# Optimization experiments

Hardware: AMD Instinct MI355X
Metric: run time of the kernel (lower is better)

Reference implementation:

```python
import jax, jax.numpy as jnp
import numpy as np

N_NODES = 50000
N_EDGES = 800000
IN_NODE = 64
IN_EDGE = 64
HIDDEN = 128
OUT_NODE = 64


def _linear_params(key, fan_in, fan_out):
    k1, k2 = jax.random.split(key)
    bound = 1.0 / np.sqrt(fan_in)
    W = jax.random.uniform(k1, (fan_out, fan_in), jnp.float32, -bound, bound)
    b = jax.random.uniform(k2, (fan_out,), jnp.float32, -bound, bound)
    return W, b


def setup_inputs() -> dict:
    key = jax.random.key(0)
    ks = jax.random.split(key, 10)
    src_node_features = jax.random.normal(ks[0], (N_NODES, IN_NODE), jnp.float32)
    edge_index = jax.random.randint(ks[1], (2, N_EDGES), 0, N_NODES, dtype=jnp.int32).astype(jnp.int64)
    edge_attr = jax.random.normal(ks[2], (N_EDGES, IN_EDGE), jnp.float32)
    u = jax.random.normal(ks[3], (1, 16), jnp.float32)
    batch = jnp.zeros((N_NODES,), jnp.int64)
    # node_mlp_1: Linear(in_node+in_edge, hidden) -> ReLU -> Linear(hidden, out)
    W1a, b1a = _linear_params(ks[4], IN_NODE + IN_EDGE, HIDDEN)
    W1b, b1b = _linear_params(ks[5], HIDDEN, OUT_NODE)
    # node_mlp_2: Linear(in_node+out, hidden) -> ReLU -> Linear(hidden, out)
    W2a, b2a = _linear_params(ks[6], IN_NODE + OUT_NODE, HIDDEN)
    W2b, b2b = _linear_params(ks[7], HIDDEN, OUT_NODE)
    # residual_combine: Linear(out+in_node, out)
    Wr, br = _linear_params(ks[8], OUT_NODE + IN_NODE, OUT_NODE)
    return {
        "src_node_features": src_node_features,
        "edge_index": edge_index,
        "edge_attr": edge_attr,
        "u": u,
        "batch": batch,
        "W1a": W1a, "b1a": b1a, "W1b": W1b, "b1b": b1b,
        "W2a": W2a, "b2a": b2a, "W2b": W2b, "b2b": b2b,
        "Wr": Wr, "br": br,
    }


def reference(src_node_features, edge_index, edge_attr, u, batch,
              W1a, b1a, W1b, b1b, W2a, b2a, W2b, b2b, Wr, br):
    n_nodes = src_node_features.shape[0]
    row, col = edge_index[0], edge_index[1]
    # gather source-node features per edge and concat with edge features: [E, in_node+in_edge]
    msg = jnp.concatenate([src_node_features[col], edge_attr], axis=1)
    # node_mlp_1
    h = jax.nn.relu(msg @ W1a.T + b1a)
    h = h @ W1b.T + b1b  # [E, out]
    # scatter_mean over destination nodes (row)
    sums = jax.ops.segment_sum(h, row, num_segments=n_nodes)
    counts = jax.ops.segment_sum(jnp.ones((h.shape[0],), h.dtype), row, num_segments=n_nodes)
    agg = sums / jnp.maximum(counts, 1.0)[:, None]  # [N, out]
    # node_mlp_2
    z = jnp.concatenate([src_node_features, agg], axis=1)
    z = jax.nn.relu(z @ W2a.T + b2a)
    z = z @ W2b.T + b2b  # [N, out]
    # residual combine
    out = jnp.concatenate([z, src_node_features], axis=1) @ Wr.T + br
    return out
```

## Files before the change

kernel.cpp:

```cpp
#include <hip/hip_runtime.h>

#define N_NODES 50000
#define N_EDGES 800000
#define HPAD 136
#define ZPAD 72
#define MAXDEG 64
#define ETILE 32

typedef __attribute__((ext_vector_type(8))) short short8;
typedef __attribute__((ext_vector_type(4))) float float4v;

__device__ __forceinline__ unsigned short f2bf(float x) {
    unsigned int u = __float_as_uint(x);
    u += 0x7fff + ((u >> 16) & 1);
    return (unsigned short)(u >> 16);
}
__device__ __forceinline__ float bf2f(unsigned short b) {
    return __uint_as_float(((unsigned int)b) << 16);
}
__device__ __forceinline__ int clampN(int v) {
    v = v < 0 ? 0 : v;
    return v >= N_NODES ? N_NODES - 1 : v;
}
__device__ __forceinline__ short8 cvt8(const float* __restrict__ p) {
    float4v f0 = *reinterpret_cast<const float4v*>(p);
    float4v f1 = *reinterpret_cast<const float4v*>(p + 4);
    short8 v;
    #pragma unroll
    for (int j = 0; j < 4; ++j) {
        v[j]     = (short)f2bf(f0[j]);
        v[j + 4] = (short)f2bf(f1[j]);
    }
    return v;
}
__device__ __forceinline__ int loadIdx(const int* __restrict__ p, long i, bool w64) {
    return w64 ? p[2 * i] : p[i];
}
__device__ __forceinline__ bool idxIs64(const int* __restrict__ p) {
    return (p[1] | p[3] | p[5] | p[7]) == 0;
}

#define OFF_W1A 0
#define OFF_W1B 16384
#define OFF_W2A 24576
#define OFF_W2B 40960
#define OFF_WR  49152
#define WBF_TOT 57344

__global__ void wcvt_kernel(const float* __restrict__ W1a, const float* __restrict__ W1b,
                            const float* __restrict__ W2a, const float* __restrict__ W2b,
                            const float* __restrict__ Wr, unsigned short* __restrict__ wbf)
{
    int i = blockIdx.x * 256 + threadIdx.x;
    if (i >= WBF_TOT) return;
    float v;
    if      (i < OFF_W1B) v = W1a[i - OFF_W1A];
    else if (i < OFF_W2A) v = W1b[i - OFF_W1B];
    else if (i < OFF_W2B) v = W2a[i - OFF_W2A];
    else if (i < OFF_WR)  v = W2b[i - OFF_W2B];
    else                  v = Wr[i - OFF_WR];
    wbf[i] = f2bf(v);
}

__global__ void scvt_kernel(const float* __restrict__ src, unsigned short* __restrict__ sbf)
{
    int i = blockIdx.x * 256 + threadIdx.x;
    sbf[i] = f2bf(src[i]);
}

__global__ __launch_bounds__(256, 2)
void edge_kernel5(const float* __restrict__ src,
                  const int* __restrict__ eidx,
                  const float* __restrict__ eattr,
                  const unsigned short* __restrict__ wbf,
                  const unsigned short* __restrict__ srcbf,
                  const float* __restrict__ b1a,
                  const float* __restrict__ b1b,
                  unsigned short* __restrict__ h,
                  int* __restrict__ cnt,
                  int* __restrict__ adj)
{
    __shared__ __align__(16) unsigned short h_lds[4][ETILE][HPAD];

    const int tid  = threadIdx.x;
    const int wave = tid >> 6;
    const int lane = tid & 63;
    const int quad = lane >> 4;
    const int lm   = lane & 15;
    const int ebase = blockIdx.x * (ETILE * 4) + wave * ETILE;

    const bool w64 = idxIs64(eidx);

    if (lane < ETILE) {
        const int e = ebase + lane;
        const int r = clampN(loadIdx(eidx, e, w64));
        const int pos = atomicAdd(&cnt[r], 1);
        if (pos < MAXDEG) adj[r * MAXDEG + pos] = e;
    }

    int col[2];
    #pragma unroll
    for (int t = 0; t < 2; ++t)
        col[t] = clampN(loadIdx(eidx, (long)N_EDGES + ebase + t * 16 + lm, w64));

    short8 a1[2][4];
    if (srcbf) {
        #pragma unroll
        for (int t = 0; t < 2; ++t) {
            #pragma unroll
            for (int s = 0; s < 2; ++s)
                a1[t][s] = *reinterpret_cast<const short8*>(
                    srcbf + (long)col[t] * 64 + s * 32 + quad * 8);
            #pragma unroll
            for (int s = 2; s < 4; ++s)
                a1[t][s] = cvt8(eattr + (long)(ebase + t * 16 + lm) * 64 + (s - 2) * 32 + quad * 8);
        }
    } else {
        #pragma unroll
        for (int t = 0; t < 2; ++t) {
            #pragma unroll
            for (int s = 0; s < 4; ++s) {
                const int kb = s * 32 + quad * 8;
                const float* p = (s < 2) ? (src + (long)col[t] * 64 + kb)
                                         : (eattr + (long)(ebase + t * 16 + lm) * 64 + (kb - 64));
                a1[t][s] = cvt8(p);
            }
        }
    }

    const unsigned short* W1a = wbf + OFF_W1A;
    const unsigned short* W1b = wbf + OFF_W1B;

    #pragma unroll
    for (int nt = 0; nt < 8; ++nt) {
        short8 bfr[4];
        #pragma unroll
        for (int s = 0; s < 4; ++s)
            bfr[s] = *reinterpret_cast<const short8*>(W1a + (nt * 16 + lm) * 128 + s * 32 + quad * 8);
        float4v acc0 = {0.f, 0.f, 0.f, 0.f};
        float4v acc1 = {0.f, 0.f, 0.f, 0.f};
        #pragma unroll
        for (int s = 0; s < 4; ++s) {
            acc0 = __builtin_amdgcn_mfma_f32_16x16x32_bf16(a1[0][s], bfr[s], acc0, 0, 0, 0);
            acc1 = __builtin_amdgcn_mfma_f32_16x16x32_bf16(a1[1][s], bfr[s], acc1, 0, 0, 0);
        }
        const float bias = b1a[nt * 16 + lm];
        #pragma unroll
        for (int r = 0; r < 4; ++r) {
            float v0 = acc0[r] + bias; v0 = v0 > 0.f ? v0 : 0.f;
            float v1 = acc1[r] + bias; v1 = v1 > 0.f ? v1 : 0.f;
            h_lds[wave][quad * 4 + r][nt * 16 + lm]      = f2bf(v0);
            h_lds[wave][16 + quad * 4 + r][nt * 16 + lm] = f2bf(v1);
        }
    }

    short8 a2[2][4];
    #pragma unroll
    for (int t = 0; t < 2; ++t)
        #pragma unroll
        for (int s = 0; s < 4; ++s)
            a2[t][s] = *reinterpret_cast<const short8*>(&h_lds[wave][t * 16 + lm][s * 32 + quad * 8]);

    #pragma unroll
    for (int nt = 0; nt < 4; ++nt) {
        short8 bfr[4];
        #pragma unroll
        for (int s = 0; s < 4; ++s)
            bfr[s] = *reinterpret_cast<const short8*>(W1b + (nt * 16 + lm) * 128 + s * 32 + quad * 8);
        float4v acc0 = {0.f, 0.f, 0.f, 0.f};
        float4v acc1 = {0.f, 0.f, 0.f, 0.f};
        #pragma unroll
        for (int s = 0; s < 4; ++s) {
            acc0 = __builtin_amdgcn_mfma_f32_16x16x32_bf16(a2[0][s], bfr[s], acc0, 0, 0, 0);
            acc1 = __builtin_amdgcn_mfma_f32_16x16x32_bf16(a2[1][s], bfr[s], acc1, 0, 0, 0);
        }
        const float bias = b1b[nt * 16 + lm];
        #pragma unroll
        for (int r = 0; r < 4; ++r) {
            h_lds[wave][quad * 4 + r][nt * 16 + lm]      = f2bf(acc0[r] + bias);
            h_lds[wave][16 + quad * 4 + r][nt * 16 + lm] = f2bf(acc1[r] + bias);
        }
    }

    const int m    = lane >> 1;
    const int half = lane & 1;
    #pragma unroll
    for (int i = 0; i < 2; ++i) {
        short8 v = *reinterpret_cast<const short8*>(&h_lds[wave][m][half * 32 + i * 16 + 0]);
        short8 w = *reinterpret_cast<const short8*>(&h_lds[wave][m][half * 32 + i * 16 + 8]);
        unsigned short* g = h + (long)(ebase + m) * 64 + half * 32 + i * 16;
        *reinterpret_cast<short8*>(g)     = v;
        *reinterpret_cast<short8*>(g + 8) = w;
    }
}

__global__ __launch_bounds__(256, 8)
void agg_kernel(const unsigned short* __restrict__ h,
                const int* __restrict__ cnt,
                const int* __restrict__ adj,
                unsigned short* __restrict__ aggbf)
{
    const int tid  = threadIdx.x;
    const int wave = tid >> 6;
    const int lane = tid & 63;
    const int g = lane >> 3;
    const int s = lane & 7;
    const int n = blockIdx.x * 4 + wave;

    const int deg  = cnt[n];
    const int degc = deg > MAXDEG ? MAXDEG : deg;
    const int* arow = adj + n * MAXDEG;

    float acc[8];
    #pragma unroll
    for (int c = 0; c < 8; ++c) acc[c] = 0.f;

    for (int j = g; j < degc; j += 8) {
        const int e = arow[j];
        short8 v = *reinterpret_cast<const short8*>(h + (long)e * 64 + s * 8);
        #pragma unroll
        for (int c = 0; c < 8; ++c) acc[c] += bf2f((unsigned short)v[c]);
    }

    #pragma unroll
    for (int m = 8; m < 64; m <<= 1) {
        #pragma unroll
        for (int c = 0; c < 8; ++c)
            acc[c] += __shfl_xor(acc[c], m, 64);
    }

    if (g == 0) {
        const float inv = 1.f / (deg > 1 ? (float)deg : 1.f);
        short8 o;
        #pragma unroll
        for (int c = 0; c < 8; ++c) o[c] = (short)f2bf(acc[c] * inv);
        *reinterpret_cast<short8*>(aggbf + (long)n * 64 + s * 8) = o;
    }
}

__global__ __launch_bounds__(256, 2)
void node_mlp_kernel(const unsigned short* __restrict__ srcbf,
                     const unsigned short* __restrict__ aggbf,
                     const unsigned short* __restrict__ wbf,
                     const float* __restrict__ b2a,
                     const float* __restrict__ b2b,
                     const float* __restrict__ br,
                     float* __restrict__ out)
{
    __shared__ __align__(16) unsigned short h_lds[4][16][HPAD];
    __shared__ __align__(16) unsigned short z_lds[4][16][ZPAD];

    const int tid  = threadIdx.x;
    const int wave = tid >> 6;
    const int lane = tid & 63;
    const int quad = lane >> 4;
    const int lm   = lane & 15;
    const int nbase = blockIdx.x * 64 + wave * 16;
    const int node_g = clampN(nbase + lm);

    short8 a1f[4];
    #pragma unroll
    for (int s = 0; s < 2; ++s)
        a1f[s] = *reinterpret_cast<const short8*>(srcbf + (long)node_g * 64 + s * 32 + quad * 8);
    #pragma unroll
    for (int s = 2; s < 4; ++s)
        a1f[s] = *reinterpret_cast<const short8*>(aggbf + (long)node_g * 64 + (s - 2) * 32 + quad * 8);

    const unsigned short* W2a = wbf + OFF_W2A;
    const unsigned short* W2b = wbf + OFF_W2B;
    const unsigned short* Wr  = wbf + OFF_WR;

    #pragma unroll
    for (int nt = 0; nt < 8; ++nt) {
        float4v acc = {0.f, 0.f, 0.f, 0.f};
        #pragma unroll
        for (int s = 0; s < 4; ++s) {
            short8 b = *reinterpret_cast<const short8*>(W2a + (nt * 16 + lm) * 128 + s * 32 + quad * 8);
            acc = __builtin_amdgcn_mfma_f32_16x16x32_bf16(a1f[s], b, acc, 0, 0, 0);
        }
        const float bias = b2a[nt * 16 + lm];
        #pragma unroll
        for (int r = 0; r < 4; ++r) {
            float v = acc[r] + bias;
            v = v > 0.f ? v : 0.f;
            h_lds[wave][quad * 4 + r][nt * 16 + lm] = f2bf(v);
        }
    }

    short8 a2f[4];
    #pragma unroll
    for (int s = 0; s < 4; ++s)
        a2f[s] = *reinterpret_cast<const short8*>(&h_lds[wave][lm][s * 32 + quad * 8]);

    #pragma unroll
    for (int nt = 0; nt < 4; ++nt) {
        float4v acc = {0.f, 0.f, 0.f, 0.f};
        #pragma unroll
        for (int s = 0; s < 4; ++s) {
            short8 b = *reinterpret_cast<const short8*>(W2b + (nt * 16 + lm) * 128 + s * 32 + quad * 8);
            acc = __builtin_amdgcn_mfma_f32_16x16x32_bf16(a2f[s], b, acc, 0, 0, 0);
        }
        const float bias = b2b[nt * 16 + lm];
        #pragma unroll
        for (int r = 0; r < 4; ++r)
            z_lds[wave][quad * 4 + r][nt * 16 + lm] = f2bf(acc[r] + bias);
    }

    short8 a3f[4];
    #pragma unroll
    for (int s = 0; s < 2; ++s)
        a3f[s] = *reinterpret_cast<const short8*>(&z_lds[wave][lm][s * 32 + quad * 8]);
    a3f[2] = a1f[0];
    a3f[3] = a1f[1];

    #pragma unroll
    for (int nt = 0; nt < 4; ++nt) {
        float4v acc = {0.f, 0.f, 0.f, 0.f};
        #pragma unroll
        for (int s = 0; s < 4; ++s) {
            short8 b = *reinterpret_cast<const short8*>(Wr + (nt * 16 + lm) * 128 + s * 32 + quad * 8);
            acc = __builtin_amdgcn_mfma_f32_16x16x32_bf16(a3f[s], b, acc, 0, 0, 0);
        }
        const float bias = br[nt * 16 + lm];
        #pragma unroll
        for (int r = 0; r < 4; ++r) {
            const int node = nbase + quad * 4 + r;
            if (node < N_NODES)
                out[(long)node * 64 + nt * 16 + lm] = acc[r] + bias;
        }
    }
}

__global__ __launch_bounds__(256, 2)
void node_kernel3(const float* __restrict__ src,
                  const unsigned short* __restrict__ srcbf,
                  const unsigned short* __restrict__ h,
                  const int* __restrict__ cnt,
                  const int* __restrict__ adj,
                  const unsigned short* __restrict__ wbf,
                  const float* __restrict__ b2a,
                  const float* __restrict__ b2b,
                  const float* __restrict__ br,
                  float* __restrict__ out)
{
    __shared__ __align__(16) unsigned short agg_lds[4][16][ZPAD];
    __shared__ __align__(16) unsigned short h_lds[4][16][HPAD];
    __shared__ __align__(16) unsigned short z_lds[4][16][ZPAD];

    const int tid  = threadIdx.x;
    const int wave = tid >> 6;
    const int lane = tid & 63;
    const int quad = lane >> 4;
    const int lm   = lane & 15;
    const int nbase = blockIdx.x * 64 + wave * 16;

    const int node_g = clampN(nbase + lm);

    const int deg  = cnt[node_g];
    const int degc = deg > MAXDEG ? MAXDEG : deg;
    const int ch0  = quad * 16;
    const int* arow = adj + node_g * MAXDEG;

    float s0[16];
    #pragma unroll
    for (int c = 0; c < 16; ++c) s0[c] = 0.f;

    int j = 0;
    for (; j + 4 <= degc; j += 4) {
        const int4 e4 = *reinterpret_cast<const int4*>(arow + j);
        const unsigned short* p0 = h + (long)e4.x * 64 + ch0;
        const unsigned short* p1 = h + (long)e4.y * 64 + ch0;
        const unsigned short* p2 = h + (long)e4.z * 64 + ch0;
        const unsigned short* p3 = h + (long)e4.w * 64 + ch0;
        short8 a0 = *reinterpret_cast<const short8*>(p0);
        short8 b0 = *reinterpret_cast<const short8*>(p0 + 8);
        short8 a1 = *reinterpret_cast<const short8*>(p1);
        short8 b1 = *reinterpret_cast<const short8*>(p1 + 8);
        short8 a2 = *reinterpret_cast<const short8*>(p2);
        short8 b2 = *reinterpret_cast<const short8*>(p2 + 8);
        short8 a3 = *reinterpret_cast<const short8*>(p3);
        short8 b3 = *reinterpret_cast<const short8*>(p3 + 8);
        #pragma unroll
        for (int c = 0; c < 8; ++c) {
            s0[c]     += bf2f((unsigned short)a0[c]) + bf2f((unsigned short)a1[c])
                       + bf2f((unsigned short)a2[c]) + bf2f((unsigned short)a3[c]);
            s0[c + 8] += bf2f((unsigned short)b0[c]) + bf2f((unsigned short)b1[c])
                       + bf2f((unsigned short)b2[c]) + bf2f((unsigned short)b3[c]);
        }
    }
    for (; j < degc; ++j) {
        const unsigned short* p = h + (long)arow[j] * 64 + ch0;
        short8 a = *reinterpret_cast<const short8*>(p);
        short8 b = *reinterpret_cast<const short8*>(p + 8);
        #pragma unroll
        for (int c = 0; c < 8; ++c) {
            s0[c]     += bf2f((unsigned short)a[c]);
            s0[c + 8] += bf2f((unsigned short)b[c]);
        }
    }
    const float inv = 1.f / (deg > 1 ? (float)deg : 1.f);

    #pragma unroll
    for (int k = 0; k < 8; ++k) {
        unsigned int pk = ((unsigned int)f2bf(s0[2 * k + 1] * inv) << 16)
                        | f2bf(s0[2 * k] * inv);
        *reinterpret_cast<unsigned int*>(&agg_lds[wave][lm][ch0 + 2 * k]) = pk;
    }

    short8 a1f[4];
    if (srcbf) {
        #pragma unroll
        for (int s = 0; s < 2; ++s)
            a1f[s] = *reinterpret_cast<const short8*>(srcbf + (long)node_g * 64 + s * 32 + quad * 8);
    } else {
        #pragma unroll
        for (int s = 0; s < 2; ++s)
            a1f[s] = cvt8(src + (long)node_g * 64 + s * 32 + quad * 8);
    }
    #pragma unroll
    for (int s = 2; s < 4; ++s)
        a1f[s] = *reinterpret_cast<const short8*>(&agg_lds[wave][lm][(s - 2) * 32 + quad * 8]);

    const unsigned short* W2a = wbf + OFF_W2A;
    const unsigned short* W2b = wbf + OFF_W2B;
    const unsigned short* Wr  = wbf + OFF_WR;

    #pragma unroll
    for (int nt = 0; nt < 8; ++nt) {
        float4v acc = {0.f, 0.f, 0.f, 0.f};
        #pragma unroll
        for (int s = 0; s < 4; ++s) {
            short8 b = *reinterpret_cast<const short8*>(W2a + (nt * 16 + lm) * 128 + s * 32 + quad * 8);
            acc = __builtin_amdgcn_mfma_f32_16x16x32_bf16(a1f[s], b, acc, 0, 0, 0);
        }
        const float bias = b2a[nt * 16 + lm];
        #pragma unroll
        for (int r = 0; r < 4; ++r) {
            float v = acc[r] + bias;
            v = v > 0.f ? v : 0.f;
            h_lds[wave][quad * 4 + r][nt * 16 + lm] = f2bf(v);
        }
    }

    short8 a2f[4];
    #pragma unroll
    for (int s = 0; s < 4; ++s)
        a2f[s] = *reinterpret_cast<const short8*>(&h_lds[wave][lm][s * 32 + quad * 8]);

    #pragma unroll
    for (int nt = 0; nt < 4; ++nt) {
        float4v acc = {0.f, 0.f, 0.f, 0.f};
        #pragma unroll
        for (int s = 0; s < 4; ++s) {
            short8 b = *reinterpret_cast<const short8*>(W2b + (nt * 16 + lm) * 128 + s * 32 + quad * 8);
            acc = __builtin_amdgcn_mfma_f32_16x16x32_bf16(a2f[s], b, acc, 0, 0, 0);
        }
        const float bias = b2b[nt * 16 + lm];
        #pragma unroll
        for (int r = 0; r < 4; ++r)
            z_lds[wave][quad * 4 + r][nt * 16 + lm] = f2bf(acc[r] + bias);
    }

    short8 a3f[4];
    #pragma unroll
    for (int s = 0; s < 2; ++s)
        a3f[s] = *reinterpret_cast<const short8*>(&z_lds[wave][lm][s * 32 + quad * 8]);
    a3f[2] = a1f[0];
    a3f[3] = a1f[1];

    #pragma unroll
    for (int nt = 0; nt < 4; ++nt) {
        float4v acc = {0.f, 0.f, 0.f, 0.f};
        #pragma unroll
        for (int s = 0; s < 4; ++s) {
            short8 b = *reinterpret_cast<const short8*>(Wr + (nt * 16 + lm) * 128 + s * 32 + quad * 8);
            acc = __builtin_amdgcn_mfma_f32_16x16x32_bf16(a3f[s], b, acc, 0, 0, 0);
        }
        const float bias = br[nt * 16 + lm];
        #pragma unroll
        for (int r = 0; r < 4; ++r) {
            const int node = nbase + quad * 4 + r;
            if (node < N_NODES)
                out[(long)node * 64 + nt * 16 + lm] = acc[r] + bias;
        }
    }
}

__global__ __launch_bounds__(256, 2)
void edge_kernel_fb(const float* __restrict__ src, const int* __restrict__ eidx,
                    const float* __restrict__ eattr, const float* __restrict__ W1a,
                    const float* __restrict__ b1a, const float* __restrict__ W1b,
                    const float* __restrict__ b1b, float* __restrict__ sums,
                    float* __restrict__ counts)
{
    __shared__ __align__(16) unsigned short h_lds[4][16][HPAD];
    const int tid = threadIdx.x, wave = tid >> 6, lane = tid & 63;
    const int quad = lane >> 4, lm = lane & 15;
    const int ebase = blockIdx.x * 64 + wave * 16;
    const bool w64 = idxIs64(eidx);
    const int e_a = ebase + lm;
    const int colv = clampN(loadIdx(eidx, (long)N_EDGES + e_a, w64));
    short8 a1[4];
    #pragma unroll
    for (int s = 0; s < 4; ++s) {
        const int kb = s * 32 + quad * 8;
        const float* p = (s < 2) ? (src + (long)colv * 64 + kb)
                                 : (eattr + (long)e_a * 64 + (kb - 64));
        a1[s] = cvt8(p);
    }
    #pragma unroll
    for (int nt = 0; nt < 8; ++nt) {
        float4v acc = {0.f, 0.f, 0.f, 0.f};
        #pragma unroll
        for (int s = 0; s < 4; ++s) {
            short8 b = cvt8(W1a + (nt * 16 + lm) * 128 + s * 32 + quad * 8);
            acc = __builtin_amdgcn_mfma_f32_16x16x32_bf16(a1[s], b, acc, 0, 0, 0);
        }
        const float bias = b1a[nt * 16 + lm];
        #pragma unroll
        for (int r = 0; r < 4; ++r) {
            float v = acc[r] + bias; v = v > 0.f ? v : 0.f;
            h_lds[wave][quad * 4 + r][nt * 16 + lm] = f2bf(v);
        }
    }
    __syncthreads();
    short8 a2[4];
    #pragma unroll
    for (int s = 0; s < 4; ++s)
        a2[s] = *reinterpret_cast<const short8*>(&h_lds[wave][lm][s * 32 + quad * 8]);
    int rowv[4];
    #pragma unroll
    for (int r = 0; r < 4; ++r)
        rowv[r] = clampN(loadIdx(eidx, ebase + quad * 4 + r, w64));
    #pragma unroll
    for (int nt = 0; nt < 4; ++nt) {
        float4v acc = {0.f, 0.f, 0.f, 0.f};
        #pragma unroll
        for (int s = 0; s < 4; ++s) {
            short8 b = cvt8(W1b + (nt * 16 + lm) * 128 + s * 32 + quad * 8);
            acc = __builtin_amdgcn_mfma_f32_16x16x32_bf16(a2[s], b, acc, 0, 0, 0);
        }
        const float bias = b1b[nt * 16 + lm];
        #pragma unroll
        for (int r = 0; r < 4; ++r)
            atomicAdd(&sums[(long)rowv[r] * 64 + nt * 16 + lm], acc[r] + bias);
    }
    if (lane < 16)
        atomicAdd(&counts[clampN(loadIdx(eidx, ebase + lane, w64))], 1.0f);
}

__global__ __launch_bounds__(256, 2)
void node_kernel_fb(const float* __restrict__ src, const float* __restrict__ sums,
                    const float* __restrict__ counts, const float* __restrict__ W2a,
                    const float* __restrict__ b2a, const float* __restrict__ W2b,
                    const float* __restrict__ b2b, const float* __restrict__ Wr,
                    const float* __restrict__ br, float* __restrict__ out)
{
    __shared__ __align__(16) unsigned short h_lds[4][16][HPAD];
    __shared__ __align__(16) unsigned short z_lds[4][16][ZPAD];
    const int tid = threadIdx.x, wave = tid >> 6, lane = tid & 63;
    const int quad = lane >> 4, lm = lane & 15;
    const int nbase = blockIdx.x * 64 + wave * 16;
    int node_a = nbase + lm;
    if (node_a >= N_NODES) node_a = N_NODES - 1;
    float cntv = counts[node_a];
    cntv = cntv > 1.f ? cntv : 1.f;
    const float inv = 1.f / cntv;
    short8 a1[4];
    #pragma unroll
    for (int s = 0; s < 2; ++s)
        a1[s] = cvt8(src + (long)node_a * 64 + s * 32 + quad * 8);
    #pragma unroll
    for (int s = 2; s < 4; ++s) {
        const int kb = s * 32 + quad * 8 - 64;
        const float4v* p = reinterpret_cast<const float4v*>(sums + (long)node_a * 64 + kb);
        float4v f0 = p[0], f1 = p[1];
        short8 v;
        #pragma unroll
        for (int jj = 0; jj < 4; ++jj) {
            v[jj] = (short)f2bf(f0[jj] * inv);
            v[jj + 4] = (short)f2bf(f1[jj] * inv);
        }
        a1[s] = v;
    }
    #pragma unroll
    for (int nt = 0; nt < 8; ++nt) {
        float4v acc = {0.f, 0.f, 0.f, 0.f};
        #pragma unroll
        for (int s = 0; s < 4; ++s) {
            short8 b = cvt8(W2a + (nt * 16 + lm) * 128 + s * 32 + quad * 8);
            acc = __builtin_amdgcn_mfma_f32_16x16x32_bf16(a1[s], b, acc, 0, 0, 0);
        }
        const float bias = b2a[nt * 16 + lm];
        #pragma unroll
        for (int r = 0; r < 4; ++r) {
            float v = acc[r] + bias; v = v > 0.f ? v : 0.f;
            h_lds[wave][quad * 4 + r][nt * 16 + lm] = f2bf(v);
        }
    }
    __syncthreads();
    short8 a2[4];
    #pragma unroll
    for (int s = 0; s < 4; ++s)
        a2[s] = *reinterpret_cast<const short8*>(&h_lds[wave][lm][s * 32 + quad * 8]);
    #pragma unroll
    for (int nt = 0; nt < 4; ++nt) {
        float4v acc = {0.f, 0.f, 0.f, 0.f};
        #pragma unroll
        for (int s = 0; s < 4; ++s) {
            short8 b = cvt8(W2b + (nt * 16 + lm) * 128 + s * 32 + quad * 8);
            acc = __builtin_amdgcn_mfma_f32_16x16x32_bf16(a2[s], b, acc, 0, 0, 0);
        }
        const float bias = b2b[nt * 16 + lm];
        #pragma unroll
        for (int r = 0; r < 4; ++r)
            z_lds[wave][quad * 4 + r][nt * 16 + lm] = f2bf(acc[r] + bias);
    }
    __syncthreads();
    short8 a3[4];
    #pragma unroll
    for (int s = 0; s < 2; ++s)
        a3[s] = *reinterpret_cast<const short8*>(&z_lds[wave][lm][s * 32 + quad * 8]);
    a3[2] = a1[0];
    a3[3] = a1[1];
    #pragma unroll
    for (int nt = 0; nt < 4; ++nt) {
        float4v acc = {0.f, 0.f, 0.f, 0.f};
        #pragma unroll
        for (int s = 0; s < 4; ++s) {
            short8 b = cvt8(Wr + (nt * 16 + lm) * 128 + s * 32 + quad * 8);
            acc = __builtin_amdgcn_mfma_f32_16x16x32_bf16(a3[s], b, acc, 0, 0, 0);
        }
        const float bias = br[nt * 16 + lm];
        #pragma unroll
        for (int r = 0; r < 4; ++r) {
            const int node = nbase + quad * 4 + r;
            if (node < N_NODES)
                out[(long)node * 64 + nt * 16 + lm] = acc[r] + bias;
        }
    }
}

extern "C" void kernel_launch(void* const* d_in, const int* in_sizes, int n_in,
                              void* d_out, int out_size, void* d_ws, size_t ws_size,
                              hipStream_t stream) {
    const long expect[15] = {
        3200000L, 1600000L, 51200000L, 16L, 50000L,
        16384L, 128L, 8192L, 64L,
        16384L, 128L, 8192L, 64L,
        8192L, 64L
    };
    const void* slot[15];
    for (int j = 0; j < 15; ++j) slot[j] = nullptr;
    {
        int i = 0;
        for (int j = 0; j < 15 && i < n_in; ++j)
            if ((long)in_sizes[i] == expect[j]) { slot[j] = d_in[i]; ++i; }
    }
    if (!slot[0] || !slot[1] || !slot[2] || !slot[5] || !slot[6] || !slot[7] ||
        !slot[8] || !slot[9] || !slot[10] || !slot[11] || !slot[12] ||
        !slot[13] || !slot[14]) {
        for (int j = 0; j < 15 && j < n_in; ++j) slot[j] = d_in[j];
    }

    const float* src   = (const float*)slot[0];
    const int*   eidx  = (const int*)slot[1];
    const float* eattr = (const float*)slot[2];
    const float* W1a = (const float*)slot[5];
    const float* b1a = (const float*)slot[6];
    const float* W1b = (const float*)slot[7];
    const float* b1b = (const float*)slot[8];
    const float* W2a = (const float*)slot[9];
    const float* b2a = (const float*)slot[10];
    const float* W2b = (const float*)slot[11];
    const float* b2b = (const float*)slot[12];
    const float* Wr  = (const float*)slot[13];
    const float* br  = (const float*)slot[14];
    float* out = (float*)d_out;

    const size_t hBytes   = (size_t)N_EDGES * 64 * sizeof(unsigned short);
    const size_t cntOff   = hBytes;
    const size_t cntBytes = (size_t)N_NODES * sizeof(int);
    const size_t adjOff   = cntOff + cntBytes;
    const size_t adjBytes = (size_t)N_NODES * MAXDEG * sizeof(int);
    const size_t wbfOff   = adjOff + adjBytes;
    const size_t needed2  = wbfOff + (size_t)WBF_TOT * sizeof(unsigned short);
    const size_t sbfOff   = needed2;
    const size_t sbfBytes = (size_t)N_NODES * 64 * sizeof(unsigned short);
    const size_t needed3  = sbfOff + sbfBytes;
    const size_t aggOff   = needed3;
    const size_t needed4  = aggOff + sbfBytes;

    if (ws_size >= needed2) {
        unsigned short* h = (unsigned short*)d_ws;
        int* cnt = (int*)((char*)d_ws + cntOff);
        int* adj = (int*)((char*)d_ws + adjOff);
        unsigned short* wbf = (unsigned short*)((char*)d_ws + wbfOff);
        unsigned short* sbf = nullptr;

        hipMemsetAsync(cnt, 0, cntBytes, stream);
        wcvt_kernel<<<(WBF_TOT + 255) / 256, 256, 0, stream>>>(W1a, W1b, W2a, W2b, Wr, wbf);
        if (ws_size >= needed3) {
            sbf = (unsigned short*)((char*)d_ws + sbfOff);
            scvt_kernel<<<(N_NODES * 64) / 256, 256, 0, stream>>>(src, sbf);
        }
        edge_kernel5<<<N_EDGES / (ETILE * 4), 256, 0, stream>>>(src, eidx, eattr, wbf, sbf,
                                                                b1a, b1b, h, cnt, adj);
        if (ws_size >= needed4 && sbf) {
            unsigned short* aggbf = (unsigned short*)((char*)d_ws + aggOff);
            agg_kernel<<<N_NODES / 4, 256, 0, stream>>>(h, cnt, adj, aggbf);
            node_mlp_kernel<<<(N_NODES + 63) / 64, 256, 0, stream>>>(sbf, aggbf, wbf,
                                                                     b2a, b2b, br, out);
        } else {
            node_kernel3<<<(N_NODES + 63) / 64, 256, 0, stream>>>(src, sbf, h, cnt, adj, wbf,
                                                                  b2a, b2b, br, out);
        }
        return;
    }

    const size_t needed_fb = ((size_t)N_NODES * 64 + N_NODES) * sizeof(float);
    if (ws_size < needed_fb) {
        hipMemsetAsync(d_out, 0, (size_t)out_size * sizeof(float), stream);
        return;
    }
    float* sums   = (float*)d_ws;
    float* counts = sums + (size_t)N_NODES * 64;
    hipMemsetAsync(d_ws, 0, needed_fb, stream);
    edge_kernel_fb<<<N_EDGES / 64, 256, 0, stream>>>(src, eidx, eattr,
                                                     W1a, b1a, W1b, b1b, sums, counts);
    node_kernel_fb<<<(N_NODES + 63) / 64, 256, 0, stream>>>(src, sums, counts,
                                                            W2a, b2a, W2b, b2b,
                                                            Wr, br, out);
}
```

Baseline: 558.5 us.

## Persistent software-pipelined edge kernel and unrolled batched-load aggregation

Replaces the one-tile-per-wave edge kernel with a persistent grid of 1024 blocks. Each wave strides over edge tiles and prefetches the next tile's gathered node and edge features and column indices while running the MLP on the current tile. Adjacency atomics are issued before the MLP and committed after it. The aggregation kernel now issues all eight neighbour loads up front instead of looping with dependent loads, which adds memory-level parallelism at the cost of extra registers. Launch bounds change to 4 blocks per SM and node_mlp_kernel is only moved, not changed.

Result: slower. 703.6 us (+26.0%).

```diff
diff --git a/kernel.cpp b/kernel.cpp
--- a/kernel.cpp
+++ b/kernel.cpp
@@ -6,6 +6,9 @@
 #define ZPAD 72
 #define MAXDEG 64
 #define ETILE 32
+#define TILES_TOTAL 25000
+#define EDGE_BLOCKS 1024
+#define EDGE_STRIDE (EDGE_BLOCKS * 4)
 
 typedef __attribute__((ext_vector_type(8))) short short8;
 typedef __attribute__((ext_vector_type(4))) float float4v;
@@ -68,6 +71,309 @@
     sbf[i] = f2bf(src[i]);
 }
 
+__global__ __launch_bounds__(256, 4)
+void edge_kernel6(const int* __restrict__ eidx,
+                  const float* __restrict__ eattr,
+                  const unsigned short* __restrict__ wbf,
+                  const unsigned short* __restrict__ srcbf,
+                  const float* __restrict__ b1a,
+                  const float* __restrict__ b1b,
+                  unsigned short* __restrict__ h,
+                  int* __restrict__ cnt,
+                  int* __restrict__ adj)
+{
+    __shared__ __align__(16) unsigned short h_lds[4][ETILE][HPAD];
+
+    const int tid  = threadIdx.x;
+    const int wave = tid >> 6;
+    const int lane = tid & 63;
+    const int quad = lane >> 4;
+    const int lm   = lane & 15;
+    const int wg   = blockIdx.x * 4 + wave;
+
+    const bool w64 = idxIs64(eidx);
+
+    const unsigned short* W1a = wbf + OFF_W1A;
+    const unsigned short* W1b = wbf + OFF_W1B;
+
+    auto loadcols = [&](int tile, int col[2]) {
+        #pragma unroll
+        for (int t = 0; t < 2; ++t)
+            col[t] = clampN(loadIdx(eidx, (long)N_EDGES + tile * ETILE + t * 16 + lm, w64));
+    };
+    auto gather = [&](int tile, const int col[2], short8 a[2][4]) {
+        #pragma unroll
+        for (int t = 0; t < 2; ++t) {
+            #pragma unroll
+            for (int s = 0; s < 2; ++s)
+                a[t][s] = *reinterpret_cast<const short8*>(
+                    srcbf + (long)col[t] * 64 + s * 32 + quad * 8);
+            #pragma unroll
+            for (int s = 2; s < 4; ++s)
+                a[t][s] = cvt8(eattr + (long)(tile * ETILE + t * 16 + lm) * 64
+                               + (s - 2) * 32 + quad * 8);
+        }
+    };
+    auto adj_issue = [&](int tile, int& pos, int& r) {
+        pos = MAXDEG; r = 0;
+        if (lane < ETILE) {
+            r = clampN(loadIdx(eidx, tile * ETILE + lane, w64));
+            pos = atomicAdd(&cnt[r], 1);
+        }
+    };
+    auto adj_commit = [&](int tile, int pos, int r) {
+        if (lane < ETILE && pos < MAXDEG)
+            adj[r * MAXDEG + pos] = tile * ETILE + lane;
+    };
+    auto mlp_store = [&](int tile, short8 a1[2][4]) {
+        const int ebase = tile * ETILE;
+        #pragma unroll
+        for (int nt = 0; nt < 8; ++nt) {
+            short8 bfr[4];
+            #pragma unroll
+            for (int s = 0; s < 4; ++s)
+                bfr[s] = *reinterpret_cast<const short8*>(
+                    W1a + (nt * 16 + lm) * 128 + s * 32 + quad * 8);
+            float4v acc0 = {0.f, 0.f, 0.f, 0.f};
+            float4v acc1 = {0.f, 0.f, 0.f, 0.f};
+            #pragma unroll
+            for (int s = 0; s < 4; ++s) {
+                acc0 = __builtin_amdgcn_mfma_f32_16x16x32_bf16(a1[0][s], bfr[s], acc0, 0, 0, 0);
+                acc1 = __builtin_amdgcn_mfma_f32_16x16x32_bf16(a1[1][s], bfr[s], acc1, 0, 0, 0);
+            }
+            const float bias = b1a[nt * 16 + lm];
+            #pragma unroll
+            for (int r = 0; r < 4; ++r) {
+                float v0 = acc0[r] + bias; v0 = v0 > 0.f ? v0 : 0.f;
+                float v1 = acc1[r] + bias; v1 = v1 > 0.f ? v1 : 0.f;
+                h_lds[wave][quad * 4 + r][nt * 16 + lm]      = f2bf(v0);
+                h_lds[wave][16 + quad * 4 + r][nt * 16 + lm] = f2bf(v1);
+            }
+        }
+        short8 a2[2][4];
+        #pragma unroll
+        for (int t = 0; t < 2; ++t)
+            #pragma unroll
+            for (int s = 0; s < 4; ++s)
+                a2[t][s] = *reinterpret_cast<const short8*>(
+                    &h_lds[wave][t * 16 + lm][s * 32 + quad * 8]);
+        #pragma unroll
+        for (int nt = 0; nt < 4; ++nt) {
+            short8 bfr[4];
+            #pragma unroll
+            for (int s = 0; s < 4; ++s)
+                bfr[s] = *reinterpret_cast<const short8*>(
+                    W1b + (nt * 16 + lm) * 128 + s * 32 + quad * 8);
+            float4v acc0 = {0.f, 0.f, 0.f, 0.f};
+            float4v acc1 = {0.f, 0.f, 0.f, 0.f};
+            #pragma unroll
+            for (int s = 0; s < 4; ++s) {
+                acc0 = __builtin_amdgcn_mfma_f32_16x16x32_bf16(a2[0][s], bfr[s], acc0, 0, 0, 0);
+                acc1 = __builtin_amdgcn_mfma_f32_16x16x32_bf16(a2[1][s], bfr[s], acc1, 0, 0, 0);
+            }
+            const float bias = b1b[nt * 16 + lm];
+            #pragma unroll
+            for (int r = 0; r < 4; ++r) {
+                h_lds[wave][quad * 4 + r][nt * 16 + lm]      = f2bf(acc0[r] + bias);
+                h_lds[wave][16 + quad * 4 + r][nt * 16 + lm] = f2bf(acc1[r] + bias);
+            }
+        }
+        const int m    = lane >> 1;
+        const int half = lane & 1;
+        #pragma unroll
+        for (int i = 0; i < 2; ++i) {
+            short8 v = *reinterpret_cast<const short8*>(&h_lds[wave][m][half * 32 + i * 16 + 0]);
+            short8 w = *reinterpret_cast<const short8*>(&h_lds[wave][m][half * 32 + i * 16 + 8]);
+            unsigned short* g = h + (long)(ebase + m) * 64 + half * 32 + i * 16;
+            *reinterpret_cast<short8*>(g)     = v;
+            *reinterpret_cast<short8*>(g + 8) = w;
+        }
+    };
+
+    short8 A[2][4], B[2][4];
+    int colN[2], colNN[2];
+
+    const int t0 = wg;
+    {
+        int cols0[2];
+        loadcols(t0, cols0);
+        int pos0, r0;
+        adj_issue(t0, pos0, r0);
+        gather(t0, cols0, A);
+        if (t0 + EDGE_STRIDE < TILES_TOTAL) loadcols(t0 + EDGE_STRIDE, colN);
+        adj_commit(t0, pos0, r0);
+    }
+
+    for (int t = t0; t < TILES_TOTAL; t += EDGE_STRIDE) {
+        const int tn  = t + EDGE_STRIDE;
+        const int tnn = t + 2 * EDGE_STRIDE;
+        if (tnn < TILES_TOTAL) loadcols(tnn, colNN);
+        int posB = MAXDEG, rB = 0;
+        if (tn < TILES_TOTAL) {
+            gather(tn, colN, B);
+            adj_issue(tn, posB, rB);
+        }
+        mlp_store(t, A);
+        if (tn < TILES_TOTAL) {
+            adj_commit(tn, posB, rB);
+            #pragma unroll
+            for (int x = 0; x < 2; ++x) {
+                #pragma unroll
+                for (int s = 0; s < 4; ++s) A[x][s] = B[x][s];
+                colN[x] = colNN[x];
+            }
+        }
+    }
+}
+
+__global__ __launch_bounds__(256, 4)
+void agg_kernel2(const unsigned short* __restrict__ h,
+                 const int* __restrict__ cnt,
+                 const int* __restrict__ adj,
+                 unsigned short* __restrict__ aggbf)
+{
+    const int tid  = threadIdx.x;
+    const int wave = tid >> 6;
+    const int lane = tid & 63;
+    const int g = lane >> 3;
+    const int s = lane & 7;
+    const int n = blockIdx.x * 4 + wave;
+
+    const int deg  = cnt[n];
+    const int degc = deg > MAXDEG ? MAXDEG : deg;
+    const int* arow = adj + n * MAXDEG;
+
+    int e[8];
+    #pragma unroll
+    for (int k = 0; k < 8; ++k) {
+        const int j = g + k * 8;
+        e[k] = (j < degc) ? arow[j] : -1;
+    }
+    short8 v[8];
+    #pragma unroll
+    for (int k = 0; k < 8; ++k) {
+        short8 z = {0, 0, 0, 0, 0, 0, 0, 0};
+        v[k] = z;
+        if (e[k] >= 0)
+            v[k] = *reinterpret_cast<const short8*>(h + (long)e[k] * 64 + s * 8);
+    }
+    float acc[8];
+    #pragma unroll
+    for (int c = 0; c < 8; ++c) acc[c] = 0.f;
+    #pragma unroll
+    for (int k = 0; k < 8; ++k)
+        #pragma unroll
+        for (int c = 0; c < 8; ++c) acc[c] += bf2f((unsigned short)v[k][c]);
+
+    #pragma unroll
+    for (int m = 8; m < 64; m <<= 1) {
+        #pragma unroll
+        for (int c = 0; c < 8; ++c)
+            acc[c] += __shfl_xor(acc[c], m, 64);
+    }
+
+    if (g == 0) {
+        const float inv = 1.f / (deg > 1 ? (float)deg : 1.f);
+        short8 o;
+        #pragma unroll
+        for (int c = 0; c < 8; ++c) o[c] = (short)f2bf(acc[c] * inv);
+        *reinterpret_cast<short8*>(aggbf + (long)n * 64 + s * 8) = o;
+    }
+}
+
+__global__ __launch_bounds__(256, 2)
+void node_mlp_kernel(const unsigned short* __restrict__ srcbf,
+                     const unsigned short* __restrict__ aggbf,
+                     const unsigned short* __restrict__ wbf,
+                     const float* __restrict__ b2a,
+                     const float* __restrict__ b2b,
+                     const float* __restrict__ br,
+                     float* __restrict__ out)
+{
+    __shared__ __align__(16) unsigned short h_lds[4][16][HPAD];
+    __shared__ __align__(16) unsigned short z_lds[4][16][ZPAD];
+
+    const int tid  = threadIdx.x;
+    const int wave = tid >> 6;
+    const int lane = tid & 63;
+    const int quad = lane >> 4;
+    const int lm   = lane & 15;
+    const int nbase = blockIdx.x * 64 + wave * 16;
+    const int node_g = clampN(nbase + lm);
+
+    short8 a1f[4];
+    #pragma unroll
+    for (int s = 0; s < 2; ++s)
+        a1f[s] = *reinterpret_cast<const short8*>(srcbf + (long)node_g * 64 + s * 32 + quad * 8);
+    #pragma unroll
+    for (int s = 2; s < 4; ++s)
+        a1f[s] = *reinterpret_cast<const short8*>(aggbf + (long)node_g * 64 + (s - 2) * 32 + quad * 8);
+
+    const unsigned short* W2a = wbf + OFF_W2A;
+    const unsigned short* W2b = wbf + OFF_W2B;
+    const unsigned short* Wr  = wbf + OFF_WR;
+
+    #pragma unroll
+    for (int nt = 0; nt < 8; ++nt) {
+        float4v acc = {0.f, 0.f, 0.f, 0.f};
+        #pragma unroll
+        for (int s = 0; s < 4; ++s) {
+            short8 b = *reinterpret_cast<const short8*>(W2a + (nt * 16 + lm) * 128 + s * 32 + quad * 8);
+            acc = __builtin_amdgcn_mfma_f32_16x16x32_bf16(a1f[s], b, acc, 0, 0, 0);
+        }
+        const float bias = b2a[nt * 16 + lm];
+        #pragma unroll
+        for (int r = 0; r < 4; ++r) {
+            float v = acc[r] + bias;
+            v = v > 0.f ? v : 0.f;
+            h_lds[wave][quad * 4 + r][nt * 16 + lm] = f2bf(v);
+        }
+    }
+
+    short8 a2f[4];
+    #pragma unroll
+    for (int s = 0; s < 4; ++s)
+        a2f[s] = *reinterpret_cast<const short8*>(&h_lds[wave][lm][s * 32 + quad * 8]);
+
+    #pragma unroll
+    for (int nt = 0; nt < 4; ++nt) {
+        float4v acc = {0.f, 0.f, 0.f, 0.f};
+        #pragma unroll
+        for (int s = 0; s < 4; ++s) {
+            short8 b = *reinterpret_cast<const short8*>(W2b + (nt * 16 + lm) * 128 + s * 32 + quad * 8);
+            acc = __builtin_amdgcn_mfma_f32_16x16x32_bf16(a2f[s], b, acc, 0, 0, 0);
+        }
+        const float bias = b2b[nt * 16 + lm];
+        #pragma unroll
+        for (int r = 0; r < 4; ++r)
+            z_lds[wave][quad * 4 + r][nt * 16 + lm] = f2bf(acc[r] + bias);
+    }
+
+    short8 a3f[4];
+    #pragma unroll
+    for (int s = 0; s < 2; ++s)
+        a3f[s] = *reinterpret_cast<const short8*>(&z_lds[wave][lm][s * 32 + quad * 8]);
+    a3f[2] = a1f[0];
+    a3f[3] = a1f[1];
+
+    #pragma unroll
+    for (int nt = 0; nt < 4; ++nt) {
+        float4v acc = {0.f, 0.f, 0.f, 0.f};
+        #pragma unroll
+        for (int s = 0; s < 4; ++s) {
+            short8 b = *reinterpret_cast<const short8*>(Wr + (nt * 16 + lm) * 128 + s * 32 + quad * 8);
+            acc = __builtin_amdgcn_mfma_f32_16x16x32_bf16(a3f[s], b, acc, 0, 0, 0);
+        }
+        const float bias = br[nt * 16 + lm];
+        #pragma unroll
+        for (int r = 0; r < 4; ++r) {
+            const int node = nbase + quad * 4 + r;
+            if (node < N_NODES)
+                out[(long)node * 64 + nt * 16 + lm] = acc[r] + bias;
+        }
+    }
+}
+
 __global__ __launch_bounds__(256, 2)
 void edge_kernel5(const float* __restrict__ src,
                   const int* __restrict__ eidx,
@@ -191,143 +497,6 @@
         unsigned short* g = h + (long)(ebase + m) * 64 + half * 32 + i * 16;
         *reinterpret_cast<short8*>(g)     = v;
         *reinterpret_cast<short8*>(g + 8) = w;
-    }
-}
-
-__global__ __launch_bounds__(256, 8)
-void agg_kernel(const unsigned short* __restrict__ h,
-                const int* __restrict__ cnt,
-                const int* __restrict__ adj,
-                unsigned short* __restrict__ aggbf)
-{
-    const int tid  = threadIdx.x;
-    const int wave = tid >> 6;
-    const int lane = tid & 63;
-    const int g = lane >> 3;
-    const int s = lane & 7;
-    const int n = blockIdx.x * 4 + wave;
-
-    const int deg  = cnt[n];
-    const int degc = deg > MAXDEG ? MAXDEG : deg;
-    const int* arow = adj + n * MAXDEG;
-
-    float acc[8];
-    #pragma unroll
-    for (int c = 0; c < 8; ++c) acc[c] = 0.f;
-
-    for (int j = g; j < degc; j += 8) {
-        const int e = arow[j];
-        short8 v = *reinterpret_cast<const short8*>(h + (long)e * 64 + s * 8);
-        #pragma unroll
-        for (int c = 0; c < 8; ++c) acc[c] += bf2f((unsigned short)v[c]);
-    }
-
-    #pragma unroll
-    for (int m = 8; m < 64; m <<= 1) {
-        #pragma unroll
-        for (int c = 0; c < 8; ++c)
-            acc[c] += __shfl_xor(acc[c], m, 64);
-    }
-
-    if (g == 0) {
-        const float inv = 1.f / (deg > 1 ? (float)deg : 1.f);
-        short8 o;
-        #pragma unroll
-        for (int c = 0; c < 8; ++c) o[c] = (short)f2bf(acc[c] * inv);
-        *reinterpret_cast<short8*>(aggbf + (long)n * 64 + s * 8) = o;
-    }
-}
-
-__global__ __launch_bounds__(256, 2)
-void node_mlp_kernel(const unsigned short* __restrict__ srcbf,
-                     const unsigned short* __restrict__ aggbf,
-                     const unsigned short* __restrict__ wbf,
-                     const float* __restrict__ b2a,
-                     const float* __restrict__ b2b,
-                     const float* __restrict__ br,
-                     float* __restrict__ out)
-{
-    __shared__ __align__(16) unsigned short h_lds[4][16][HPAD];
-    __shared__ __align__(16) unsigned short z_lds[4][16][ZPAD];
-
-    const int tid  = threadIdx.x;
-    const int wave = tid >> 6;
-    const int lane = tid & 63;
-    const int quad = lane >> 4;
-    const int lm   = lane & 15;
-    const int nbase = blockIdx.x * 64 + wave * 16;
-    const int node_g = clampN(nbase + lm);
-
-    short8 a1f[4];
-    #pragma unroll
-    for (int s = 0; s < 2; ++s)
-        a1f[s] = *reinterpret_cast<const short8*>(srcbf + (long)node_g * 64 + s * 32 + quad * 8);
-    #pragma unroll
-    for (int s = 2; s < 4; ++s)
-        a1f[s] = *reinterpret_cast<const short8*>(aggbf + (long)node_g * 64 + (s - 2) * 32 + quad * 8);
-
-    const unsigned short* W2a = wbf + OFF_W2A;
-    const unsigned short* W2b = wbf + OFF_W2B;
-    const unsigned short* Wr  = wbf + OFF_WR;
-
-    #pragma unroll
-    for (int nt = 0; nt < 8; ++nt) {
-        float4v acc = {0.f, 0.f, 0.f, 0.f};
-        #pragma unroll
-        for (int s = 0; s < 4; ++s) {
-            short8 b = *reinterpret_cast<const short8*>(W2a + (nt * 16 + lm) * 128 + s * 32 + quad * 8);
-            acc = __builtin_amdgcn_mfma_f32_16x16x32_bf16(a1f[s], b, acc, 0, 0, 0);
-        }
-        const float bias = b2a[nt * 16 + lm];
-        #pragma unroll
-        for (int r = 0; r < 4; ++r) {
-            float v = acc[r] + bias;
-            v = v > 0.f ? v : 0.f;
-            h_lds[wave][quad * 4 + r][nt * 16 + lm] = f2bf(v);
-        }
-    }
-
-    short8 a2f[4];
-    #pragma unroll
-    for (int s = 0; s < 4; ++s)
-        a2f[s] = *reinterpret_cast<const short8*>(&h_lds[wave][lm][s * 32 + quad * 8]);
-
-    #pragma unroll
-    for (int nt = 0; nt < 4; ++nt) {
-        float4v acc = {0.f, 0.f, 0.f, 0.f};
-        #pragma unroll
-        for (int s = 0; s < 4; ++s) {
-            short8 b = *reinterpret_cast<const short8*>(W2b + (nt * 16 + lm) * 128 + s * 32 + quad * 8);
-            acc = __builtin_amdgcn_mfma_f32_16x16x32_bf16(a2f[s], b, acc, 0, 0, 0);
-        }
-        const float bias = b2b[nt * 16 + lm];
-        #pragma unroll
-        for (int r = 0; r < 4; ++r)
-            z_lds[wave][quad * 4 + r][nt * 16 + lm] = f2bf(acc[r] + bias);
-    }
-
-    short8 a3f[4];
-    #pragma unroll
-    for (int s = 0; s < 2; ++s)
-        a3f[s] = *reinterpret_cast<const short8*>(&z_lds[wave][lm][s * 32 + quad * 8]);
-    a3f[2] = a1f[0];
-    a3f[3] = a1f[1];
-
-    #pragma unroll
-    for (int nt = 0; nt < 4; ++nt) {
-        float4v acc = {0.f, 0.f, 0.f, 0.f};
-        #pragma unroll
-        for (int s = 0; s < 4; ++s) {
-            short8 b = *reinterpret_cast<const short8*>(Wr + (nt * 16 + lm) * 128 + s * 32 + quad * 8);
-            acc = __builtin_amdgcn_mfma_f32_16x16x32_bf16(a3f[s], b, acc, 0, 0, 0);
-        }
-        const float bias = br[nt * 16 + lm];
-        #pragma unroll
-        for (int r = 0; r < 4; ++r) {
-            const int node = nbase + quad * 4 + r;
-            if (node < N_NODES)
-                out[(long)node * 64 + nt * 16 + lm] = acc[r] + bias;
-        }
     }
 }
 
@@ -704,11 +873,18 @@
             sbf = (unsigned short*)((char*)d_ws + sbfOff);
             scvt_kernel<<<(N_NODES * 64) / 256, 256, 0, stream>>>(src, sbf);
         }
-        edge_kernel5<<<N_EDGES / (ETILE * 4), 256, 0, stream>>>(src, eidx, eattr, wbf, sbf,
-                                                                b1a, b1b, h, cnt, adj);
+
+        if (sbf) {
+            edge_kernel6<<<EDGE_BLOCKS, 256, 0, stream>>>(eidx, eattr, wbf, sbf,
+                                                          b1a, b1b, h, cnt, adj);
+        } else {
+            edge_kernel5<<<N_EDGES / (ETILE * 4), 256, 0, stream>>>(src, eidx, eattr, wbf, sbf,
+                                                                    b1a, b1b, h, cnt, adj);
+        }
+
         if (ws_size >= needed4 && sbf) {
             unsigned short* aggbf = (unsigned short*)((char*)d_ws + aggOff);
-            agg_kernel<<<N_NODES / 4, 256, 0, stream>>>(h, cnt, adj, aggbf);
+            agg_kernel2<<<N_NODES / 4, 256, 0, stream>>>(h, cnt, adj, aggbf);
             node_mlp_kernel<<<(N_NODES + 63) / 64, 256, 0, stream>>>(sbf, aggbf, wbf,
                                                                      b2a, b2b, br, out);
         } else {
```
